# Kernel optimization log

Hardware: AMD Instinct MI355X
Metric: run time of the kernel (lower is better)

## Reference

```python
import jax, jax.numpy as jnp
import numpy as np

PARENT_LIST = [0, 0, 1, 2, 3, 4, 5, 6, 7, 8, 8, 3, 11, 12, 13, 14, 15, 15, 0, 18, 19, 20, 0, 22, 23, 24, 3]
J, D, H, L, DFF = 27, 512, 8, 6, 2048
DH = D // H
RADIUS = 0.1
B, N = 64, 2048
NEG = -1e9  # large finite negative: exp underflows to exactly 0 in fp32, grad-safe


def _topo_mask():
    m = np.full((J, J), NEG, dtype=np.float32)
    for c, p in enumerate(PARENT_LIST):
        m[c, c] = 0.0
        if c != p:
            m[c, p] = 0.0
            m[p, c] = 0.0
    return jnp.asarray(m)


def _radius_scales():
    s = np.ones(J, dtype=np.float32)
    s[[0, 1, 2, 3, 18, 22]] = 0.6
    s[[9, 10, 16, 17, 20, 21, 24, 25, 26]] = 1.5
    return jnp.asarray(s).reshape(1, J, 1)


def _ln(x, s, b):
    mu = jnp.mean(x, -1, keepdims=True)
    v = jnp.mean((x - mu) ** 2, -1, keepdims=True)
    return (x - mu) * jax.lax.rsqrt(v + 1e-5) * s + b


def _mha(q_in, k_in, v_in, qkv_w, qkv_b, out_w, out_b, add_mask):
    Bq, Q, _ = q_in.shape
    S = k_in.shape[1]
    q = (q_in @ qkv_w[:, :D] + qkv_b[:D]).reshape(Bq, Q, H, DH)
    k = (k_in @ qkv_w[:, D:2 * D] + qkv_b[D:2 * D]).reshape(Bq, S, H, DH)
    v = (v_in @ qkv_w[:, 2 * D:] + qkv_b[2 * D:]).reshape(Bq, S, H, DH)
    scores = jnp.einsum('bqhd,bkhd->bhqk', q, k) * np.float32(1.0 / np.sqrt(DH))
    attn = jax.nn.softmax(scores + add_mask, axis=-1)
    o = jnp.einsum('bhqk,bkhd->bqhd', attn, v).reshape(Bq, Q, D)
    return o @ out_w + out_b


def setup_inputs() -> dict:
    key = jax.random.key(0)
    ks = iter(jax.random.split(key, 40))
    def w(shape, scale=0.02):
        return jax.random.normal(next(ks), shape, jnp.float32) * scale
    return dict(
        x_t=jax.random.normal(next(ks), (B, J, 3), jnp.float32),
        t=jax.random.uniform(next(ks), (B, 1), jnp.float32),
        coarse_pose=jax.random.normal(next(ks), (B, J, 3), jnp.float32),
        radar_pc=jax.random.normal(next(ks), (B, N, 6), jnp.float32),
        pc_w=w((6, D)), pc_b=jnp.zeros(D),
        coarse_w=w((3, D)), coarse_b=jnp.zeros(D),
        state_w=w((3, D)), state_b=jnp.zeros(D),
        jid_emb=w((J, D), 1.0),
        dop_w1=w((1, 64)), dop_b1=jnp.zeros(64),
        dop_w2=w((64, D)), dop_b2=jnp.zeros(D),
        time_w1=w((1, D)), time_b1=jnp.zeros(D),
        time_w2=w((D, D)), time_b2=jnp.zeros(D),
        mod_w1=w((D, 2 * D)), mod_b1=jnp.zeros(2 * D),
        mod_w2=w((2 * D, 2 * D)), mod_b2=jnp.zeros(2 * D),
        diff_w=w((2 * D, D)), diff_b=jnp.zeros(D),
        vel_w=w((D, 3)), vel_b=jnp.zeros(3),
        sa_qkv_w=w((L, D, 3 * D)), sa_qkv_b=jnp.zeros((L, 3 * D)),
        sa_out_w=w((L, D, D)), sa_out_b=jnp.zeros((L, D)),
        ca_qkv_w=w((L, D, 3 * D)), ca_qkv_b=jnp.zeros((L, 3 * D)),
        ca_out_w=w((L, D, D)), ca_out_b=jnp.zeros((L, D)),
        ff1_w=w((L, D, DFF)), ff1_b=jnp.zeros((L, DFF)),
        ff2_w=w((L, DFF, D)), ff2_b=jnp.zeros((L, D)),
        ln1_s=jnp.ones((L, D)), ln1_b=jnp.zeros((L, D)),
        ln2_s=jnp.ones((L, D)), ln2_b=jnp.zeros((L, D)),
        ln3_s=jnp.ones((L, D)), ln3_b=jnp.zeros((L, D)),
    )


def reference(x_t, t, coarse_pose, radar_pc, pc_w, pc_b, coarse_w, coarse_b,
              state_w, state_b, jid_emb, dop_w1, dop_b1, dop_w2, dop_b2,
              time_w1, time_b1, time_w2, time_b2, mod_w1, mod_b1, mod_w2, mod_b2,
              diff_w, diff_b, vel_w, vel_b,
              sa_qkv_w, sa_qkv_b, sa_out_w, sa_out_b,
              ca_qkv_w, ca_qkv_b, ca_out_w, ca_out_b,
              ff1_w, ff1_b, ff2_w, ff2_b,
              ln1_s, ln1_b, ln2_s, ln2_b, ln3_s, ln3_b):
    p_idx = jnp.asarray(PARENT_LIST)
    topo = _topo_mask()          # [J,J] additive
    scales = _radius_scales()    # [1,J,1]
    pc_xyz = radar_pc[:, :, :3]
    pc_dop = radar_pc[:, :, 3:4]
    raw_memory = radar_pc @ pc_w + pc_b                               # [B,N,D]
    # euclidean distance via norm expansion (cdist p=2)
    d2 = (jnp.sum(x_t ** 2, -1)[:, :, None] + jnp.sum(pc_xyz ** 2, -1)[:, None, :]
          - 2.0 * jnp.einsum('bjc,bnc->bjn', x_t, pc_xyz))
    dist = jnp.sqrt(jnp.maximum(d2, 0.0))                             # [B,J,N]
    ar = scales * RADIUS                                              # [1,J,1]
    sig = ar / 2.0
    dw = jnp.exp(-dist ** 2 / (2.0 * sig ** 2))                       # [B,J,N]
    pi = jnp.max(dw, axis=1, keepdims=True)                           # [B,1,N]
    memory = raw_memory * jnp.swapaxes(pi, 1, 2)                      # [B,N,D]
    dop_feat = jax.nn.silu(pc_dop @ dop_w1 + dop_b1) @ dop_w2 + dop_b2
    denom = jnp.sum(dw, -1, keepdims=True) + 1e-6
    h_dop = jnp.einsum('bjn,bnd->bjd', dw, dop_feat) / denom
    h_coarse = coarse_pose @ coarse_w + coarse_b
    h_time = (jax.nn.silu(t @ time_w1 + time_b1) @ time_w2 + time_b2)[:, None, :]
    h_state = x_t @ state_w + state_b
    h_parent = h_state[:, p_idx, :]
    h_struct = jnp.concatenate([h_state, h_parent], -1) @ diff_w + diff_b
    query = h_coarse + h_time + h_dop + h_state + h_struct + jid_emb[None]
    mod = jax.nn.silu(h_state @ mod_w1 + mod_b1) @ mod_w2 + mod_b2
    shift, scale = jnp.split(mod, 2, axis=-1)
    query = query * (1.0 + scale) + shift
    # radius mask with nearest-point rescue
    smask = dist > ar
    min_idx = jnp.argmin(dist, axis=-1)                               # [B,J]
    rescue = jnp.arange(dist.shape[-1])[None, None, :] != min_idx[:, :, None]
    smask = jnp.where(jnp.all(smask, -1, keepdims=True), rescue, smask)
    mem_bias = jnp.where(smask, NEG, 0.0)[:, None, :, :]              # [B,1,J,N]
    tgt_bias = topo[None, None]                                       # [1,1,J,J]
    x = query
    for l in range(L):  # norm_first TransformerDecoderLayer, relu FFN, no dropout
        h = _ln(x, ln1_s[l], ln1_b[l])
        x = x + _mha(h, h, h, sa_qkv_w[l], sa_qkv_b[l], sa_out_w[l], sa_out_b[l], tgt_bias)
        h = _ln(x, ln2_s[l], ln2_b[l])
        x = x + _mha(h, memory, memory, ca_qkv_w[l], ca_qkv_b[l], ca_out_w[l], ca_out_b[l], mem_bias)
        h = _ln(x, ln3_s[l], ln3_b[l])
        x = x + jax.nn.relu(h @ ff1_w[l] + ff1_b[l]) @ ff2_w[l] + ff2_b[l]
    return x @ vel_w + vel_b
```

## Files before the change

kernel.cpp:

```cpp
#include <hip/hip_runtime.h>

#define J 27
#define D 512
#define H 8
#define DH 64
#define NLAYER 6
#define DFF 2048
#define NB 64
#define NP 2048
#define CAP 128
#define GCH 16
#define GPTS 128
#define NEGF -1000000000.0f

typedef unsigned short u16;
typedef __attribute__((ext_vector_type(8))) __bf16 bf16x8;
typedef __attribute__((ext_vector_type(4))) float f32x4;

__constant__ int c_parent[J] = {0,0,1,2,3,4,5,6,7,8,8,3,11,12,13,14,15,15,0,18,19,20,0,22,23,24,3};
__constant__ float c_scale[J] = {0.6f,0.6f,0.6f,0.6f,1.f,1.f,1.f,1.f,1.f,1.5f,1.5f,1.f,1.f,1.f,1.f,1.f,
                                 1.5f,1.5f,0.6f,1.f,1.5f,1.5f,0.6f,1.f,1.5f,1.5f,1.5f};

__device__ __forceinline__ float siluf(float x){ return x/(1.f+expf(-x)); }

__device__ __forceinline__ u16 f2bf(float f){
  union { float f; unsigned u; } x; x.f = f;
  unsigned r = x.u + 0x7FFFu + ((x.u >> 16) & 1u);
  return (u16)(r >> 16);
}

__global__ void k_perj(const float* __restrict__ x_t, const float* __restrict__ pc,
                       float* __restrict__ denom_sum, int* __restrict__ rescue,
                       int* __restrict__ allm, unsigned int* __restrict__ bitmap){
  int bj = blockIdx.x; int b = bj / J, j = bj % J;
  int t = threadIdx.x;
  float x0 = x_t[(b*J+j)*3+0];
  float x1 = x_t[(b*J+j)*3+1];
  float x2 = x_t[(b*J+j)*3+2];
  float sx = x0*x0+x1*x1+x2*x2;
  float ar = c_scale[j]*0.1f;
  float sig = ar*0.5f;
  float twos2 = 2.f*sig*sig;
  float sum = 0.f, bmin = 3.4e38f; int bidx = NP; int any = 0;
  for (int n = t; n < NP; n += 256){
    const float* p = pc + ((size_t)b*NP + n)*6;
    float p0=p[0], p1=p[1], p2=p[2];
    float d2 = sx + (p0*p0+p1*p1+p2*p2) - 2.f*(x0*p0+x1*p1+x2*p2);
    float dist = sqrtf(fmaxf(d2, 0.f));
    sum += expf(-(dist*dist)/twos2);
    if (dist < bmin){ bmin = dist; bidx = n; }
    if (dist <= ar){ any = 1; atomicOr(&bitmap[b*(NP/32)+(n>>5)], 1u<<(n&31)); }
  }
  __shared__ float ssum[256]; __shared__ float smin[256];
  __shared__ int sidx[256]; __shared__ int sany[256];
  ssum[t]=sum; smin[t]=bmin; sidx[t]=bidx; sany[t]=any;
  __syncthreads();
  for (int s = 128; s > 0; s >>= 1){
    if (t < s){
      ssum[t] += ssum[t+s];
      if (smin[t+s] < smin[t] || (smin[t+s]==smin[t] && sidx[t+s] < sidx[t])){ smin[t]=smin[t+s]; sidx[t]=sidx[t+s]; }
      sany[t] |= sany[t+s];
    }
    __syncthreads();
  }
  if (t == 0){
    denom_sum[bj] = ssum[0];
    rescue[bj] = sidx[0];
    allm[bj] = sany[0] ? 0 : 1;
    if (!sany[0]) atomicOr(&bitmap[b*(NP/32)+(sidx[0]>>5)], 1u<<(sidx[0]&31));
  }
}

__global__ void k_compact(const unsigned int* __restrict__ bitmap, int* __restrict__ act_idx,
                          int* __restrict__ act_cnt){
  int b = blockIdx.x; int t = threadIdx.x;
  unsigned int w = bitmap[b*(NP/32)+t];
  int c = __popc(w);
  int off = c;
  for (int s = 1; s < 64; s <<= 1){
    int v = __shfl_up(off, s);
    if (t >= s) off += v;
  }
  int total = __shfl(off, 63);
  off -= c;
  int base = off;
  for (int bit = 0; bit < 32; ++bit){
    if (w & (1u<<bit)){
      if (base < CAP) act_idx[b*CAP+base] = t*32+bit;
      base++;
    }
  }
  if (t == 0) act_cnt[b] = total > CAP ? CAP : total;
}

__global__ void k_scan(const int* __restrict__ act_cnt, int* __restrict__ act_off,
                       int* __restrict__ act_total){
  if (threadIdx.x == 0){
    int s = 0;
    for (int b = 0; b < NB; ++b){ act_off[b] = s; s += act_cnt[b]; }
    act_total[0] = s;
  }
}

__launch_bounds__(256)
__global__ void k_gpart(const float* __restrict__ x_t, const float* __restrict__ pc,
                        const float* __restrict__ dop_w1, const float* __restrict__ dop_b1,
                        float* __restrict__ Gp){
  int b = blockIdx.x, ch = blockIdx.y; int t = threadIdx.x;
  __shared__ float sx[J*3];
  __shared__ float w1s[64], b1s[64];
  __shared__ float spx[GPTS], spy[GPTS], spz[GPTS], sdp[GPTS];
  __shared__ u16 hidT[64*128];
  __shared__ u16 dwsA[32*128];
  if (t < J*3) sx[t] = x_t[b*J*3 + t];
  if (t < 64){ w1s[t] = dop_w1[t]; b1s[t] = dop_b1[t]; }
  int n0 = ch*GPTS;
  if (t < GPTS){
    const float* p = pc + ((size_t)b*NP + n0 + t)*6;
    float2 f0 = *(const float2*)p;
    float2 f1 = *(const float2*)(p+2);
    spx[t]=f0.x; spy[t]=f0.y; spz[t]=f1.x; sdp[t]=f1.y;
  }
  __syncthreads();
  {
    int h = t & 63, pb = (t>>6)*32;
    float w1 = w1s[h], b1 = b1s[h];
    char* base = (char*)hidT;
    #pragma unroll
    for (int m = 0; m < 16; ++m){
      float v0 = siluf(sdp[pb+2*m]*w1 + b1);
      float v1 = siluf(sdp[pb+2*m+1]*w1 + b1);
      unsigned pk = (unsigned)f2bf(v0) | ((unsigned)f2bf(v1) << 16);
      int off = (h*256 + pb*2 + 4*m) ^ ((h&7)<<4);
      *(unsigned*)(base + off) = pk;
    }
  }
  {
    int j = t & 31, pb = (t>>5)*16;
    if (j < J){
      float x0=sx[j*3], x1=sx[j*3+1], x2=sx[j*3+2];
      float sxx = x0*x0+x1*x1+x2*x2;
      float sig = c_scale[j]*0.05f;
      float inv2 = 1.f/(2.f*sig*sig);
      char* base = (char*)dwsA;
      #pragma unroll
      for (int m = 0; m < 8; ++m){
        float v[2];
        #pragma unroll
        for (int u = 0; u < 2; ++u){
          int p = pb + 2*m + u;
          float p0=spx[p], p1=spy[p], p2=spz[p];
          float d2 = sxx + (p0*p0+p1*p1+p2*p2) - 2.f*(x0*p0+x1*p1+x2*p2);
          float dist = sqrtf(fmaxf(d2, 0.f));
          v[u] = expf(-(dist*dist)*inv2);
        }
        unsigned pk = (unsigned)f2bf(v[0]) | ((unsigned)f2bf(v[1]) << 16);
        int off = (j*256 + pb*2 + 4*m) ^ ((j&7)<<4);
        *(unsigned*)(base + off) = pk;
      }
    }
  }
  __syncthreads();
  int lane = t & 63, wv = t >> 6;
  int h0 = wv * 16;
  int fr = lane & 15, fkb = (lane>>4)*16;
  f32x4 acc[2] = {};
  #pragma unroll
  for (int ks = 0; ks < 4; ++ks){
    bf16x8 bfrag;
    {
      int row = h0 + fr;
      int adr = (row*256 + ks*64 + fkb) ^ ((row&7)<<4);
      bfrag = *(const bf16x8*)((char*)hidT + adr);
    }
    #pragma unroll
    for (int m = 0; m < 2; ++m){
      int row = m*16 + fr;
      int adr = (row*256 + ks*64 + fkb) ^ ((row&7)<<4);
      bf16x8 afrag = *(const bf16x8*)((char*)dwsA + adr);
      acc[m] = __builtin_amdgcn_mfma_f32_16x16x32_bf16(afrag, bfrag, acc[m], 0,0,0);
    }
  }
  float* out = Gp + ((size_t)(b*GCH+ch))*J*64;
  int er = (lane>>4)*4, ec = lane&15;
  #pragma unroll
  for (int m = 0; m < 2; ++m){
    #pragma unroll
    for (int q = 0; q < 4; ++q){
      int j = m*16 + er + q;
      if (j < J) out[j*64 + h0 + ec] = acc[m][q];
    }
  }
}

__global__ void k_gred(const float* __restrict__ Gp, float* __restrict__ G){
  int idx = blockIdx.x*256 + threadIdx.x;
  int bj = idx >> 6, h = idx & 63;
  int b = bj / J, j = bj % J;
  float s = 0.f;
  #pragma unroll
  for (int c = 0; c < GCH; ++c) s += Gp[((size_t)(b*GCH+c)*J + j)*64 + h];
  G[idx] = s;
}

__launch_bounds__(256)
__global__ void k_hdop2(const float* __restrict__ G, const float* __restrict__ dop_w2,
                        const float* __restrict__ dop_b2, const float* __restrict__ denom_sum,
                        float* __restrict__ h_dop){
  int b = blockIdx.x, half = blockIdx.y;
  int t = threadIdx.x;
  int d = half*256 + t;
  __shared__ float sG[J*64];
  __shared__ float sS[J], sI[J];
  for (int e = t; e < J*64; e += 256) sG[e] = G[(size_t)b*J*64 + e];
  if (t < J){ float S = denom_sum[b*J+t]; sS[t] = S; sI[t] = 1.f/(S+1e-6f); }
  __syncthreads();
  float acc[J];
  #pragma unroll
  for (int j = 0; j < J; ++j) acc[j] = 0.f;
  for (int h = 0; h < 64; ++h){
    float wv = dop_w2[h*D + d];
    #pragma unroll
    for (int j = 0; j < J; ++j) acc[j] += sG[j*64+h]*wv;
  }
  float b2 = dop_b2[d];
  #pragma unroll
  for (int j = 0; j < J; ++j)
    h_dop[(size_t)(b*J+j)*D + d] = (acc[j] + sS[j]*b2)*sI[j];
}

__global__ void k_stage1(const float* __restrict__ x_t, const float* __restrict__ state_w,
                         const float* __restrict__ state_b,
                         const float* __restrict__ coarse, const float* __restrict__ coarse_w,
                         const float* __restrict__ coarse_b,
                         const float* __restrict__ t_in, const float* __restrict__ time_w1,
                         const float* __restrict__ time_b1,
                         float* __restrict__ h_state, u16* __restrict__ hsh,
                         float* __restrict__ h_coarse, u16* __restrict__ thh){
  const int RD = NB*J*D;
  int idx = blockIdx.x*256 + threadIdx.x;
  if (idx < RD){
    int r = idx / D, d = idx % D;
    const float* ir = x_t + r*3;
    float v = ir[0]*state_w[d] + ir[1]*state_w[D+d] + ir[2]*state_w[2*D+d] + state_b[d];
    h_state[idx] = v;
    hsh[idx] = f2bf(v);
  } else if (idx < 2*RD){
    int k = idx - RD;
    int r = k / D, d = k % D;
    const float* ir = coarse + r*3;
    h_coarse[k] = ir[0]*coarse_w[d] + ir[1]*coarse_w[D+d] + ir[2]*coarse_w[2*D+d] + coarse_b[d];
  } else if (idx < 2*RD + NB*D){
    int k = idx - 2*RD;
    int b = k / D, d = k % D;
    float v = siluf(t_in[b]*time_w1[d] + time_b1[d]);
    thh[k] = f2bf(v);
  }
}

__global__ void k_hs2(const float* __restrict__ h_state, u16* __restrict__ oh){
  int idx = blockIdx.x*256 + threadIdx.x;
  if (idx >= NB*J*2*D) return;
  int r = idx / (2*D), c = idx % (2*D);
  int b = r / J, j = r % J;
  float v;
  if (c < D) v = h_state[(size_t)r*D + c];
  else       v = h_state[((size_t)(b*J) + c_parent[j])*D + (c-D)];
  oh[idx] = f2bf(v);
}

__global__ void k_query(const float* __restrict__ h_coarse, const float* __restrict__ h_time,
                        const float* __restrict__ h_dop, const float* __restrict__ h_state,
                        const float* __restrict__ hstruct, const float* __restrict__ jid,
                        const float* __restrict__ mod2, float* __restrict__ x){
  int idx = blockIdx.x*256 + threadIdx.x;
  if (idx >= NB*J*D) return;
  int r = idx / D, d = idx % D;
  int b = r / J, j = r % J;
  float q = h_coarse[idx] + h_time[b*D+d] + h_dop[idx] + h_state[idx] + hstruct[idx] + jid[j*D+d];
  float shift = mod2[(size_t)r*2*D + d];
  float scale = mod2[(size_t)r*2*D + D + d];
  x[idx] = q*(1.f+scale) + shift;
}

__global__ void k_memact(const float* __restrict__ x_t, const float* __restrict__ pc,
                         const float* __restrict__ pc_w, const float* __restrict__ pc_b,
                         const int* __restrict__ act_idx, const int* __restrict__ act_cnt,
                         const int* __restrict__ act_off, u16* __restrict__ mh){
  int b = blockIdx.x / CAP, i = blockIdx.x % CAP;
  if (i >= act_cnt[b]) return;
  int n = act_idx[b*CAP+i];
  int t = threadIdx.x;
  __shared__ float sdw[J];
  __shared__ float spi;
  const float* p = pc + ((size_t)b*NP+n)*6;
  if (t < J){
    float x0 = x_t[(b*J+t)*3+0], x1 = x_t[(b*J+t)*3+1], x2 = x_t[(b*J+t)*3+2];
    float p0=p[0], p1=p[1], p2=p[2];
    float d2 = (x0*x0+x1*x1+x2*x2) + (p0*p0+p1*p1+p2*p2) - 2.f*(x0*p0+x1*p1+x2*p2);
    float dist = sqrtf(fmaxf(d2,0.f));
    float sig = c_scale[t]*0.05f;
    sdw[t] = expf(-(dist*dist)/(2.f*sig*sig));
  }
  __syncthreads();
  if (t == 0){ float m = sdw[0]; for (int k = 1; k < J; ++k) m = fmaxf(m, sdw[k]); spi = m; }
  __syncthreads();
  float pi = spi;
  float p0=p[0],p1=p[1],p2=p[2],p3=p[3],p4=p[4],p5=p[5];
  int g = act_off[b] + i;
  for (int d = t; d < D; d += 128){
    float acc = pc_b[d] + p0*pc_w[d] + p1*pc_w[D+d] + p2*pc_w[2*D+d]
              + p3*pc_w[3*D+d] + p4*pc_w[4*D+d] + p5*pc_w[5*D+d];
    mh[(size_t)g*D + d] = f2bf(acc * pi);
  }
}

__launch_bounds__(256)
__global__ void k_wconv(const float* __restrict__ W, u16* __restrict__ Wt, int K, int N){
  int k0 = blockIdx.x*64, n0 = blockIdx.y*64;
  size_t zo = (size_t)blockIdx.z*K*N;
  __shared__ float tile[64][65];
  int t = threadIdx.x;
  #pragma unroll
  for (int i = 0; i < 16; ++i){
    int idx = i*256 + t; int k = idx>>6, n = idx&63;
    tile[k][n] = W[zo + (size_t)(k0+k)*N + n0+n];
  }
  __syncthreads();
  #pragma unroll
  for (int i = 0; i < 8; ++i){
    int idx = i*256 + t; int n = idx>>5, kp = (idx&31)*2;
    unsigned pk = (unsigned)f2bf(tile[kp][n]) | ((unsigned)f2bf(tile[kp+1][n])<<16);
    *(unsigned*)&Wt[zo + (size_t)(n0+n)*K + k0+kp] = pk;
  }
}

template<int TM>
__launch_bounds__(256)
__global__ void k_gemm(const u16* __restrict__ Ag, const u16* __restrict__ Bt,
                       const float* __restrict__ bias, const float* __restrict__ res,
                       float* __restrict__ Cf, u16* __restrict__ Ch,
                       int M, int N, int K, int act,
                       const int* __restrict__ Mdev, int ntx){
  int Meff = Mdev ? *Mdev : M;
  int nwg = gridDim.x;
  int q8 = nwg>>3, r8 = nwg&7;
  int xcd = blockIdx.x&7, loc = blockIdx.x>>3;
  int wg = (xcd < r8 ? xcd*(q8+1) : r8*(q8+1)+(xcd-r8)*q8) + loc;
  int row0 = (wg % ntx)*TM, col0 = (wg / ntx)*64;
  if (row0 >= Meff) return;

  constexpr int MFR = TM/32;
  constexpr int RW  = TM/2;
  __shared__ u16 sA[TM*64], sB[64*64];
  int t = threadIdx.x;
  int lane = t&63, w = t>>6, wr = w>>1, wc = w&1;
  int sm = t>>3, kc = t&7;
  const u16* pA1 = Ag + (size_t)(row0+sm)*K + kc*8;
  const u16* pA2 = (TM==64) ? Ag + (size_t)(row0+sm+32)*K + kc*8 : pA1;
  const u16* pB1 = Bt + (size_t)(col0+sm)*K + kc*8;
  const u16* pB2 = Bt + (size_t)(col0+sm+32)*K + kc*8;
  int o1 = (sm*128 + kc*16) ^ ((sm&7)<<4);
  int o2 = ((sm+32)*128 + kc*16) ^ ((sm&7)<<4);
  uint4 ra1, ra2, rb1, rb2;
  auto gload = [&](int kt){
    ra1 = *(const uint4*)(pA1 + kt);
    if constexpr (TM==64) ra2 = *(const uint4*)(pA2 + kt);
    rb1 = *(const uint4*)(pB1 + kt);
    rb2 = *(const uint4*)(pB2 + kt);
  };
  auto stage = [&](){
    *(uint4*)((char*)sA + o1) = ra1;
    if constexpr (TM==64) *(uint4*)((char*)sA + o2) = ra2;
    *(uint4*)((char*)sB + o1) = rb1;
    *(uint4*)((char*)sB + o2) = rb2;
  };
  int fr = lane&15, fkb = (lane>>4)*16;
  f32x4 acc[MFR][2] = {};
  gload(0);
  stage();
  __syncthreads();
  for (int kt = 0; kt < K; kt += 64){
    bool nxt = kt + 64 < K;
    if (nxt) gload(kt + 64);
    #pragma unroll
    for (int kk = 0; kk < 2; ++kk){
      bf16x8 af[MFR], bf[2];
      #pragma unroll
      for (int m = 0; m < MFR; ++m){
        int row = wr*RW + m*16 + fr;
        int adr = (row*128 + kk*64 + fkb) ^ ((row&7)<<4);
        af[m] = *(const bf16x8*)((char*)sA + adr);
      }
      #pragma unroll
      for (int n = 0; n < 2; ++n){
        int rowb = wc*32 + n*16 + fr;
        int adr = (rowb*128 + kk*64 + fkb) ^ ((rowb&7)<<4);
        bf[n] = *(const bf16x8*)((char*)sB + adr);
      }
      #pragma unroll
      for (int m = 0; m < MFR; ++m)
        #pragma unroll
        for (int n = 0; n < 2; ++n)
          acc[m][n] = __builtin_amdgcn_mfma_f32_16x16x32_bf16(af[m], bf[n], acc[m][n], 0,0,0);
    }
    if (nxt){
      __syncthreads();
      stage();
      __syncthreads();
    }
  }
  int er = (lane>>4)*4, ec = lane&15;
  #pragma unroll
  for (int m = 0; m < MFR; ++m){
    #pragma unroll
    for (int qq = 0; qq < 4; ++qq){
      int r = row0 + wr*RW + m*16 + er + qq;
      if (r >= Meff) continue;
      #pragma unroll
      for (int n = 0; n < 2; ++n){
        int c = col0 + wc*32 + n*16 + ec;
        float v = acc[m][n][qq] + bias[c];
        if (res) v += res[(size_t)r*N + c];
        if (act == 1) v = v/(1.f+expf(-v));
        else if (act == 2) v = fmaxf(v, 0.f);
        if (Cf) Cf[(size_t)r*N + c] = v;
        if (Ch) Ch[(size_t)r*N + c] = f2bf(v);
      }
    }
  }
}

__global__ void k_ln(const float* __restrict__ x, const float* __restrict__ s,
                     const float* __restrict__ bb, u16* __restrict__ oh){
  int r = blockIdx.x; int t = threadIdx.x;
  const float* xr = x + (size_t)r*D;
  float v0 = xr[t], v1 = xr[t+256];
  __shared__ float red[256];
  red[t] = v0+v1; __syncthreads();
  for (int st = 128; st > 0; st >>= 1){ if (t < st) red[t] += red[t+st]; __syncthreads(); }
  float mu = red[0]/(float)D;
  __syncthreads();
  float d0 = v0-mu, d1 = v1-mu;
  red[t] = d0*d0 + d1*d1; __syncthreads();
  for (int st = 128; st > 0; st >>= 1){ if (t < st) red[t] += red[t+st]; __syncthreads(); }
  float var = red[0]/(float)D;
  float rs = rsqrtf(var + 1e-5f);
  oh[(size_t)r*D + t]       = f2bf(d0*rs*s[t]       + bb[t]);
  oh[(size_t)r*D + t + 256] = f2bf(d1*rs*s[t+256]   + bb[t+256]);
}

__launch_bounds__(256)
__global__ void k_selfattn(const float* __restrict__ qkv, u16* __restrict__ oh){
  int bh = blockIdx.x; int b = bh / H, h = bh % H;
  int t = threadIdx.x;
  __shared__ float qs[J*DH], ks[J*DH], vs[J*DH];
  __shared__ float ss[J*J];
  for (int e = t; e < J*DH; e += 256){
    int j = e/DH, d = e%DH;
    const float* base = qkv + (size_t)(b*J+j)*1536 + h*DH + d;
    qs[e] = base[0]; ks[e] = base[512]; vs[e] = base[1024];
  }
  __syncthreads();
  for (int e = t; e < J*J; e += 256){
    int qj = e/J, kk = e%J;
    float acc = 0.f;
    for (int d = 0; d < DH; ++d) acc += qs[qj*DH+d]*ks[kk*DH+d];
    float bias = (qj==kk || c_parent[qj]==kk || c_parent[kk]==qj) ? 0.f : NEGF;
    ss[e] = acc*0.125f + bias;
  }
  __syncthreads();
  if (t < J){
    float m = -3.4e38f;
    for (int k = 0; k < J; ++k) m = fmaxf(m, ss[t*J+k]);
    float sum = 0.f;
    for (int k = 0; k < J; ++k){ float e_ = expf(ss[t*J+k]-m); ss[t*J+k] = e_; sum += e_; }
    float inv = 1.f/sum;
    for (int k = 0; k < J; ++k) ss[t*J+k] *= inv;
  }
  __syncthreads();
  for (int e = t; e < J*DH; e += 256){
    int j = e/DH, d = e%DH;
    float acc = 0.f;
    for (int k = 0; k < J; ++k) acc += ss[j*J+k]*vs[k*DH+d];
    oh[(size_t)(b*J+j)*D + h*DH + d] = f2bf(acc);
  }
}

__launch_bounds__(256)
__global__ void k_crossattn(const float* __restrict__ qbuf, const float* __restrict__ kv_act,
                            const float* __restrict__ x_t, const float* __restrict__ pc,
                            const int* __restrict__ act_idx, const int* __restrict__ act_cnt,
                            const int* __restrict__ act_off, const int* __restrict__ rescue,
                            const int* __restrict__ allm, u16* __restrict__ oh){
  int bh = blockIdx.x; int b = bh / H, h = bh % H;
  int t = threadIdx.x;
  int cnt = act_cnt[b], off = act_off[b];
  __shared__ float qs[J*DH];
  __shared__ float ks[CAP*DH];
  __shared__ float pxyz[CAP*3];
  __shared__ float sx[J*3];
  __shared__ int sn[CAP];
  __shared__ float ss[J*CAP];
  if (t < J*3) sx[t] = x_t[b*J*3+t];
  for (int e = t; e < J*DH; e += 256)
    qs[e] = qbuf[(size_t)(b*J + e/DH)*D + h*DH + (e%DH)];
  for (int e = t; e < cnt*DH; e += 256){
    int i = e/DH, d = e%DH;
    ks[e] = kv_act[(size_t)(off+i)*1024 + h*DH + d];
  }
  for (int i = t; i < cnt; i += 256){
    int n = act_idx[b*CAP+i]; sn[i] = n;
    const float* p = pc + ((size_t)b*NP+n)*6;
    pxyz[i*3] = p[0]; pxyz[i*3+1] = p[1]; pxyz[i*3+2] = p[2];
  }
  __syncthreads();
  for (int e = t; e < J*cnt; e += 256){
    int j = e/cnt, i = e%cnt;
    float acc = 0.f;
    for (int d = 0; d < DH; ++d) acc += qs[j*DH+d]*ks[i*DH+d];
    float bias;
    if (allm[b*J+j]) bias = (sn[i] == rescue[b*J+j]) ? 0.f : NEGF;
    else {
      float x0=sx[j*3], x1=sx[j*3+1], x2=sx[j*3+2];
      float p0=pxyz[i*3], p1=pxyz[i*3+1], p2=pxyz[i*3+2];
      float d2 = (x0*x0+x1*x1+x2*x2) + (p0*p0+p1*p1+p2*p2) - 2.f*(x0*p0+x1*p1+x2*p2);
      float dist = sqrtf(fmaxf(d2,0.f));
      float ar = c_scale[j]*0.1f;
      bias = (dist > ar) ? NEGF : 0.f;
    }
    ss[j*CAP+i] = acc*0.125f + bias;
  }
  __syncthreads();
  if (t < J){
    float m = -3.4e38f;
    for (int i = 0; i < cnt; ++i) m = fmaxf(m, ss[t*CAP+i]);
    float sum = 0.f;
    for (int i = 0; i < cnt; ++i){ float e_ = expf(ss[t*CAP+i]-m); ss[t*CAP+i] = e_; sum += e_; }
    float inv = 1.f/sum;
    for (int i = 0; i < cnt; ++i) ss[t*CAP+i] *= inv;
  }
  __syncthreads();
  for (int e = t; e < J*DH; e += 256){
    int j = e/DH, d = e%DH;
    float acc = 0.f;
    for (int i = 0; i < cnt; ++i)
      acc += ss[j*CAP+i]*kv_act[(size_t)(off+i)*1024 + 512 + h*DH + d];
    oh[(size_t)(b*J+j)*D + h*DH + d] = f2bf(acc);
  }
}

__global__ void k_vel(const float* __restrict__ x, const float* __restrict__ vel_w,
                      const float* __restrict__ vel_b, float* __restrict__ out){
  int r = blockIdx.x; int t = threadIdx.x;
  int c = t >> 6; int lane = t & 63;
  float acc = 0.f;
  const float* xr = x + (size_t)r*D;
  for (int d = lane; d < D; d += 64) acc += xr[d]*vel_w[d*3+c];
  for (int s = 32; s > 0; s >>= 1) acc += __shfl_down(acc, s);
  if (lane == 0) out[r*3+c] = acc + vel_b[c];
}

static void gemm(const u16* Ah, const u16* Bt, const float* bias,
                 const float* res, float* Cf, u16* Ch,
                 int M, int N, int K, int act, const int* Mdev, int tm, hipStream_t s){
  if (tm == 32){
    int ntx = (M + 31) / 32;
    k_gemm<32><<<ntx*(N/64), 256, 0, s>>>(Ah, Bt, bias, res, Cf, Ch, M, N, K, act, Mdev, ntx);
  } else {
    int ntx = (M + 63) / 64;
    k_gemm<64><<<ntx*(N/64), 256, 0, s>>>(Ah, Bt, bias, res, Cf, Ch, M, N, K, act, Mdev, ntx);
  }
}

extern "C" void kernel_launch(void* const* d_in, const int* in_sizes, int n_in,
                              void* d_out, int out_size, void* d_ws, size_t ws_size,
                              hipStream_t stream){
  const float* x_t        = (const float*)d_in[0];
  const float* t_in       = (const float*)d_in[1];
  const float* coarse     = (const float*)d_in[2];
  const float* radar      = (const float*)d_in[3];
  const float* pc_w       = (const float*)d_in[4];
  const float* pc_b       = (const float*)d_in[5];
  const float* coarse_w   = (const float*)d_in[6];
  const float* coarse_b   = (const float*)d_in[7];
  const float* state_w    = (const float*)d_in[8];
  const float* state_b    = (const float*)d_in[9];
  const float* jid_emb    = (const float*)d_in[10];
  const float* dop_w1     = (const float*)d_in[11];
  const float* dop_b1     = (const float*)d_in[12];
  const float* dop_w2     = (const float*)d_in[13];
  const float* dop_b2     = (const float*)d_in[14];
  const float* time_w1    = (const float*)d_in[15];
  const float* time_b1    = (const float*)d_in[16];
  const float* time_w2    = (const float*)d_in[17];
  const float* time_b2    = (const float*)d_in[18];
  const float* mod_w1     = (const float*)d_in[19];
  const float* mod_b1     = (const float*)d_in[20];
  const float* mod_w2     = (const float*)d_in[21];
  const float* mod_b2     = (const float*)d_in[22];
  const float* diff_w     = (const float*)d_in[23];
  const float* diff_b     = (const float*)d_in[24];
  const float* vel_w      = (const float*)d_in[25];
  const float* vel_b      = (const float*)d_in[26];
  const float* sa_qkv_w   = (const float*)d_in[27];
  const float* sa_qkv_b   = (const float*)d_in[28];
  const float* sa_out_w   = (const float*)d_in[29];
  const float* sa_out_b   = (const float*)d_in[30];
  const float* ca_qkv_w   = (const float*)d_in[31];
  const float* ca_qkv_b   = (const float*)d_in[32];
  const float* ca_out_w   = (const float*)d_in[33];
  const float* ca_out_b   = (const float*)d_in[34];
  const float* ff1_w      = (const float*)d_in[35];
  const float* ff1_b      = (const float*)d_in[36];
  const float* ff2_w      = (const float*)d_in[37];
  const float* ff2_b      = (const float*)d_in[38];
  const float* ln1_s      = (const float*)d_in[39];
  const float* ln1_b      = (const float*)d_in[40];
  const float* ln2_s      = (const float*)d_in[41];
  const float* ln2_b      = (const float*)d_in[42];
  const float* ln3_s      = (const float*)d_in[43];
  const float* ln3_b      = (const float*)d_in[44];
  (void)in_sizes; (void)n_in; (void)out_size; (void)ws_size;

  const int R = NB*J;

  char* wp = (char*)d_ws;
  auto alloc = [&](size_t bytes)->void*{
    void* r = (void*)wp;
    wp += (bytes + 255) & ~(size_t)255;
    return r;
  };
  float*        denom_sum = (float*)alloc(R*4);
  int*          rescue    = (int*)  alloc(R*4);
  int*          allm      = (int*)  alloc(R*4);
  unsigned int* bitmap    = (unsigned int*)alloc(NB*(NP/32)*4);
  int*          act_idx   = (int*)  alloc(NB*CAP*4);
  int*          act_cnt   = (int*)  alloc(NB*4);
  int*          act_off   = (int*)  alloc(NB*4);
  int*          act_total = (int*)  alloc(64);
  float* Gp       = (float*)alloc((size_t)NB*GCH*J*64*4);
  float* G        = (float*)alloc((size_t)R*64*4);
  float* h_dop    = (float*)alloc((size_t)R*D*4);
  float* h_state  = (float*)alloc((size_t)R*D*4);
  float* h_coarse = (float*)alloc((size_t)R*D*4);
  float* hstruct  = (float*)alloc((size_t)R*D*4);
  float* xres     = (float*)alloc((size_t)R*D*4);
  float* qbuf     = (float*)alloc((size_t)R*D*4);
  float* h_time   = (float*)alloc((size_t)NB*D*4);
  float* mod2     = (float*)alloc((size_t)R*2*D*4);
  float* qkv      = (float*)alloc((size_t)R*3*D*4);
  float* kv_act   = (float*)alloc((size_t)NB*CAP*2*D*4);
  u16* hsh   = (u16*)alloc((size_t)R*D*2);
  u16* hbufh = (u16*)alloc((size_t)R*D*2);
  u16* attnoh= (u16*)alloc((size_t)R*D*2);
  u16* ffhh  = (u16*)alloc((size_t)R*DFF*2);
  u16* mah   = (u16*)alloc((size_t)NB*CAP*D*2);
  u16* time_w2t = (u16*)alloc((size_t)512*512*2);
  u16* mod_w1t  = (u16*)alloc((size_t)1024*512*2);
  u16* mod_w2t  = (u16*)alloc((size_t)1024*1024*2);
  u16* diff_wt  = (u16*)alloc((size_t)512*1024*2);
  u16* sa_qkv_t = (u16*)alloc((size_t)NLAYER*1536*512*2);
  u16* sa_out_t = (u16*)alloc((size_t)NLAYER*512*512*2);
  u16* ca_qkv_t = (u16*)alloc((size_t)NLAYER*1536*512*2);
  u16* ca_out_t = (u16*)alloc((size_t)NLAYER*512*512*2);
  u16* ff1_t    = (u16*)alloc((size_t)NLAYER*2048*512*2);
  u16* ff2_t    = (u16*)alloc((size_t)NLAYER*512*2048*2);
  u16* thh   = attnoh;
  u16* mod1h = ffhh;
  u16* hs2h  = (u16*)kv_act;

  k_wconv<<<dim3(8, 8, 1),  256, 0, stream>>>(time_w2, time_w2t, 512, 512);
  k_wconv<<<dim3(8, 16, 1), 256, 0, stream>>>(mod_w1, mod_w1t, 512, 1024);
  k_wconv<<<dim3(16, 16, 1),256, 0, stream>>>(mod_w2, mod_w2t, 1024, 1024);
  k_wconv<<<dim3(16, 8, 1), 256, 0, stream>>>(diff_w, diff_wt, 1024, 512);
  k_wconv<<<dim3(8, 24, NLAYER), 256, 0, stream>>>(sa_qkv_w, sa_qkv_t, 512, 1536);
  k_wconv<<<dim3(8, 8, NLAYER),  256, 0, stream>>>(sa_out_w, sa_out_t, 512, 512);
  k_wconv<<<dim3(8, 24, NLAYER), 256, 0, stream>>>(ca_qkv_w, ca_qkv_t, 512, 1536);
  k_wconv<<<dim3(8, 8, NLAYER),  256, 0, stream>>>(ca_out_w, ca_out_t, 512, 512);
  k_wconv<<<dim3(8, 32, NLAYER), 256, 0, stream>>>(ff1_w, ff1_t, 512, 2048);
  k_wconv<<<dim3(32, 8, NLAYER), 256, 0, stream>>>(ff2_w, ff2_t, 2048, 512);

  hipMemsetAsync(bitmap, 0, NB*(NP/32)*4, stream);
  k_perj<<<R, 256, 0, stream>>>(x_t, radar, denom_sum, rescue, allm, bitmap);
  k_compact<<<NB, 64, 0, stream>>>(bitmap, act_idx, act_cnt);
  k_scan<<<1, 64, 0, stream>>>(act_cnt, act_off, act_total);
  k_gpart<<<dim3(NB, GCH), 256, 0, stream>>>(x_t, radar, dop_w1, dop_b1, Gp);
  k_gred<<<R*64/256, 256, 0, stream>>>(Gp, G);
  k_hdop2<<<dim3(NB, 2), 256, 0, stream>>>(G, dop_w2, dop_b2, denom_sum, h_dop);

  k_stage1<<<(2*R*D + NB*D + 255)/256, 256, 0, stream>>>(
      x_t, state_w, state_b, coarse, coarse_w, coarse_b, t_in, time_w1, time_b1,
      h_state, hsh, h_coarse, thh);
  gemm(thh, time_w2t, time_b2, nullptr, h_time, nullptr, NB, 512, 512, 0, nullptr, 32, stream);
  gemm(hsh, mod_w1t, mod_b1, nullptr, nullptr, mod1h, R, 1024, 512, 1, nullptr, 32, stream);
  gemm(mod1h, mod_w2t, mod_b2, nullptr, mod2, nullptr, R, 1024, 1024, 0, nullptr, 32, stream);
  k_hs2<<<(R*2*D+255)/256, 256, 0, stream>>>(h_state, hs2h);
  gemm(hs2h, diff_wt, diff_b, nullptr, hstruct, nullptr, R, 512, 1024, 0, nullptr, 32, stream);
  k_query<<<(R*D+255)/256, 256, 0, stream>>>(h_coarse, h_time, h_dop, h_state, hstruct,
                                             jid_emb, mod2, xres);
  k_memact<<<NB*CAP, 128, 0, stream>>>(x_t, radar, pc_w, pc_b, act_idx, act_cnt, act_off, mah);

  for (int l = 0; l < NLAYER; ++l){
    k_ln<<<R, 256, 0, stream>>>(xres, ln1_s + l*D, ln1_b + l*D, hbufh);
    gemm(hbufh, sa_qkv_t + (size_t)l*1536*512, sa_qkv_b + l*1536, nullptr,
         qkv, nullptr, R, 1536, 512, 0, nullptr, 32, stream);
    k_selfattn<<<NB*H, 256, 0, stream>>>(qkv, attnoh);
    gemm(attnoh, sa_out_t + (size_t)l*512*512, sa_out_b + l*D, xres,
         xres, nullptr, R, 512, 512, 0, nullptr, 32, stream);

    k_ln<<<R, 256, 0, stream>>>(xres, ln2_s + l*D, ln2_b + l*D, hbufh);
    gemm(hbufh, ca_qkv_t + (size_t)l*1536*512, ca_qkv_b + l*1536, nullptr,
         qbuf, nullptr, R, 512, 512, 0, nullptr, 32, stream);
    gemm(mah, ca_qkv_t + (size_t)l*1536*512 + (size_t)512*512, ca_qkv_b + l*1536 + 512,
         nullptr, kv_act, nullptr, NB*CAP, 1024, 512, 0, act_total, 64, stream);
    k_crossattn<<<NB*H, 256, 0, stream>>>(qbuf, kv_act, x_t, radar, act_idx, act_cnt,
                                          act_off, rescue, allm, attnoh);
    gemm(attnoh, ca_out_t + (size_t)l*512*512, ca_out_b + l*D, xres,
         xres, nullptr, R, 512, 512, 0, nullptr, 32, stream);

    k_ln<<<R, 256, 0, stream>>>(xres, ln3_s + l*D, ln3_b + l*D, hbufh);
    gemm(hbufh, ff1_t + (size_t)l*2048*512, ff1_b + l*DFF, nullptr,
         nullptr, ffhh, R, 2048, 512, 2, nullptr, 32, stream);
    gemm(ffhh, ff2_t + (size_t)l*512*2048, ff2_b + l*D, xres,
         xres, nullptr, R, 512, 2048, 0, nullptr, 32, stream);
  }

  k_vel<<<R, 192, 0, stream>>>(xres, vel_w, vel_b, (float*)d_out);
}
```

Before: 1.062 ms.

## Double-buffer GEMM LDS, fuse small launches, merge cross-attn projections

The GEMM kernel now double-buffers its LDS tiles, which removes one barrier per K-step so the next tile's store overlaps the current MFMA work. The ten weight-conversion launches become one table-driven kernel, and the Gp reduction is folded into k_hdop2, which drops a launch and a temporary buffer. The cross-attention Q projection and the KV projection run in a single dual-GEMM launch. The self-attention QKV and FF1 GEMMs switch to 64-row tiles. LDS use per GEMM block doubles, which may reduce occupancy.

```diff
diff --git a/kernel.cpp b/kernel.cpp
--- a/kernel.cpp
+++ b/kernel.cpp
@@ -193,18 +193,8 @@
   }
 }
 
-__global__ void k_gred(const float* __restrict__ Gp, float* __restrict__ G){
-  int idx = blockIdx.x*256 + threadIdx.x;
-  int bj = idx >> 6, h = idx & 63;
-  int b = bj / J, j = bj % J;
-  float s = 0.f;
-  #pragma unroll
-  for (int c = 0; c < GCH; ++c) s += Gp[((size_t)(b*GCH+c)*J + j)*64 + h];
-  G[idx] = s;
-}
-
 __launch_bounds__(256)
-__global__ void k_hdop2(const float* __restrict__ G, const float* __restrict__ dop_w2,
+__global__ void k_hdop2(const float* __restrict__ Gp, const float* __restrict__ dop_w2,
                         const float* __restrict__ dop_b2, const float* __restrict__ denom_sum,
                         float* __restrict__ h_dop){
   int b = blockIdx.x, half = blockIdx.y;
@@ -212,7 +202,12 @@
   int d = half*256 + t;
   __shared__ float sG[J*64];
   __shared__ float sS[J], sI[J];
-  for (int e = t; e < J*64; e += 256) sG[e] = G[(size_t)b*J*64 + e];
+  for (int e = t; e < J*64; e += 256){
+    float s = 0.f;
+    #pragma unroll
+    for (int c = 0; c < GCH; ++c) s += Gp[(size_t)(b*GCH+c)*J*64 + e];
+    sG[e] = s;
+  }
   if (t < J){ float S = denom_sum[b*J+t]; sS[t] = S; sI[t] = 1.f/(S+1e-6f); }
   __syncthreads();
   float acc[J];
@@ -315,51 +310,63 @@
   }
 }
 
+struct WcD { const float* src; u16* dst; int K; int N; int tk; int tn; int L; int start; };
+struct WcTab { WcD d[10]; };
 __launch_bounds__(256)
-__global__ void k_wconv(const float* __restrict__ W, u16* __restrict__ Wt, int K, int N){
-  int k0 = blockIdx.x*64, n0 = blockIdx.y*64;
-  size_t zo = (size_t)blockIdx.z*K*N;
+__global__ void k_wconv_all(WcTab tab){
+  int tid = blockIdx.x;
+  WcD w = tab.d[0];
+  #pragma unroll
+  for (int i = 0; i < 10; ++i){
+    int end = tab.d[i].start + tab.d[i].tk*tab.d[i].tn*tab.d[i].L;
+    if (tid >= tab.d[i].start && tid < end) w = tab.d[i];
+  }
+  int local = tid - w.start;
+  int per = w.tk*w.tn;
+  int l = local / per, rem = local % per;
+  int k0 = (rem % w.tk)*64, n0 = (rem / w.tk)*64;
+  size_t zo = (size_t)l*w.K*w.N;
   __shared__ float tile[64][65];
   int t = threadIdx.x;
   #pragma unroll
   for (int i = 0; i < 16; ++i){
     int idx = i*256 + t; int k = idx>>6, n = idx&63;
-    tile[k][n] = W[zo + (size_t)(k0+k)*N + n0+n];
+    tile[k][n] = w.src[zo + (size_t)(k0+k)*w.N + n0+n];
   }
   __syncthreads();
   #pragma unroll
   for (int i = 0; i < 8; ++i){
     int idx = i*256 + t; int n = idx>>5, kp = (idx&31)*2;
     unsigned pk = (unsigned)f2bf(tile[kp][n]) | ((unsigned)f2bf(tile[kp+1][n])<<16);
-    *(unsigned*)&Wt[zo + (size_t)(n0+n)*K + k0+kp] = pk;
-  }
-}
+    *(unsigned*)&w.dst[zo + (size_t)(n0+n)*w.K + k0+kp] = pk;
+  }
+}
+
+struct GemmArgs {
+  const u16* Ag; const u16* Bt; const float* bias; const float* res;
+  float* Cf; u16* Ch; int M, N, K, act; const int* Mdev; int ntx; int nwg;
+};
 
 template<int TM>
-__launch_bounds__(256)
-__global__ void k_gemm(const u16* __restrict__ Ag, const u16* __restrict__ Bt,
-                       const float* __restrict__ bias, const float* __restrict__ res,
-                       float* __restrict__ Cf, u16* __restrict__ Ch,
-                       int M, int N, int K, int act,
-                       const int* __restrict__ Mdev, int ntx){
-  int Meff = Mdev ? *Mdev : M;
-  int nwg = gridDim.x;
-  int q8 = nwg>>3, r8 = nwg&7;
-  int xcd = blockIdx.x&7, loc = blockIdx.x>>3;
+__device__ __forceinline__ void gemm_body(const GemmArgs g, int bid, char* smem){
+  int Meff = g.Mdev ? *g.Mdev : g.M;
+  int q8 = g.nwg>>3, r8 = g.nwg&7;
+  int xcd = bid&7, loc = bid>>3;
   int wg = (xcd < r8 ? xcd*(q8+1) : r8*(q8+1)+(xcd-r8)*q8) + loc;
-  int row0 = (wg % ntx)*TM, col0 = (wg / ntx)*64;
+  int row0 = (wg % g.ntx)*TM, col0 = (wg / g.ntx)*64;
   if (row0 >= Meff) return;
-
-  constexpr int MFR = TM/32;
-  constexpr int RW  = TM/2;
-  __shared__ u16 sA[TM*64], sB[64*64];
+  constexpr int ABUF = TM*64*2;
+  constexpr int BBUF = 64*64*2;
+  char* sAb[2] = { smem, smem + ABUF };
+  char* sBb[2] = { smem + 2*ABUF, smem + 2*ABUF + BBUF };
   int t = threadIdx.x;
   int lane = t&63, w = t>>6, wr = w>>1, wc = w&1;
   int sm = t>>3, kc = t&7;
-  const u16* pA1 = Ag + (size_t)(row0+sm)*K + kc*8;
-  const u16* pA2 = (TM==64) ? Ag + (size_t)(row0+sm+32)*K + kc*8 : pA1;
-  const u16* pB1 = Bt + (size_t)(col0+sm)*K + kc*8;
-  const u16* pB2 = Bt + (size_t)(col0+sm+32)*K + kc*8;
+  int K = g.K, N = g.N;
+  const u16* pA1 = g.Ag + (size_t)(row0+sm)*K + kc*8;
+  const u16* pA2 = (TM==64) ? g.Ag + (size_t)(row0+sm+32)*K + kc*8 : pA1;
+  const u16* pB1 = g.Bt + (size_t)(col0+sm)*K + kc*8;
+  const u16* pB2 = g.Bt + (size_t)(col0+sm+32)*K + kc*8;
   int o1 = (sm*128 + kc*16) ^ ((sm&7)<<4);
   int o2 = ((sm+32)*128 + kc*16) ^ ((sm&7)<<4);
   uint4 ra1, ra2, rb1, rb2;
@@ -369,17 +376,20 @@
     rb1 = *(const uint4*)(pB1 + kt);
     rb2 = *(const uint4*)(pB2 + kt);
   };
-  auto stage = [&](){
-    *(uint4*)((char*)sA + o1) = ra1;
-    if constexpr (TM==64) *(uint4*)((char*)sA + o2) = ra2;
-    *(uint4*)((char*)sB + o1) = rb1;
-    *(uint4*)((char*)sB + o2) = rb2;
+  auto stage = [&](int bf_){
+    *(uint4*)(sAb[bf_] + o1) = ra1;
+    if constexpr (TM==64) *(uint4*)(sAb[bf_] + o2) = ra2;
+    *(uint4*)(sBb[bf_] + o1) = rb1;
+    *(uint4*)(sBb[bf_] + o2) = rb2;
   };
+  constexpr int MFR = TM/32;
+  constexpr int RW  = TM/2;
   int fr = lane&15, fkb = (lane>>4)*16;
   f32x4 acc[MFR][2] = {};
   gload(0);
-  stage();
-  __syncthreads();
+  stage(0);
+  __syncthreads();
+  int cur = 0;
   for (int kt = 0; kt < K; kt += 64){
     bool nxt = kt + 64 < K;
     if (nxt) gload(kt + 64);
@@ -390,13 +400,13 @@
       for (int m = 0; m < MFR; ++m){
         int row = wr*RW + m*16 + fr;
         int adr = (row*128 + kk*64 + fkb) ^ ((row&7)<<4);
-        af[m] = *(const bf16x8*)((char*)sA + adr);
+        af[m] = *(const bf16x8*)(sAb[cur] + adr);
       }
       #pragma unroll
       for (int n = 0; n < 2; ++n){
         int rowb = wc*32 + n*16 + fr;
         int adr = (rowb*128 + kk*64 + fkb) ^ ((rowb&7)<<4);
-        bf[n] = *(const bf16x8*)((char*)sB + adr);
+        bf[n] = *(const bf16x8*)(sBb[cur] + adr);
       }
       #pragma unroll
       for (int m = 0; m < MFR; ++m)
@@ -405,9 +415,9 @@
           acc[m][n] = __builtin_amdgcn_mfma_f32_16x16x32_bf16(af[m], bf[n], acc[m][n], 0,0,0);
     }
     if (nxt){
+      stage(cur^1);
       __syncthreads();
-      stage();
-      __syncthreads();
+      cur ^= 1;
     }
   }
   int er = (lane>>4)*4, ec = lane&15;
@@ -420,15 +430,30 @@
       #pragma unroll
       for (int n = 0; n < 2; ++n){
         int c = col0 + wc*32 + n*16 + ec;
-        float v = acc[m][n][qq] + bias[c];
-        if (res) v += res[(size_t)r*N + c];
-        if (act == 1) v = v/(1.f+expf(-v));
-        else if (act == 2) v = fmaxf(v, 0.f);
-        if (Cf) Cf[(size_t)r*N + c] = v;
-        if (Ch) Ch[(size_t)r*N + c] = f2bf(v);
+        float v = acc[m][n][qq] + g.bias[c];
+        if (g.res) v += g.res[(size_t)r*N + c];
+        if (g.act == 1) v = v/(1.f+expf(-v));
+        else if (g.act == 2) v = fmaxf(v, 0.f);
+        if (g.Cf) g.Cf[(size_t)r*N + c] = v;
+        if (g.Ch) g.Ch[(size_t)r*N + c] = f2bf(v);
       }
     }
   }
+}
+
+template<int TM>
+__launch_bounds__(256)
+__global__ void k_gemm(GemmArgs g){
+  constexpr int SZ = 2*(TM*64*2) + 2*(64*64*2);
+  __shared__ __align__(16) char smem[SZ];
+  gemm_body<TM>(g, blockIdx.x, smem);
+}
+
+__launch_bounds__(256)
+__global__ void k_gemm_dual(GemmArgs ga, GemmArgs gb){
+  __shared__ __align__(16) char smem[32768];
+  if ((int)blockIdx.x < ga.nwg) gemm_body<32>(ga, blockIdx.x, smem);
+  else                          gemm_body<64>(gb, blockIdx.x - ga.nwg, smem);
 }
 
 __global__ void k_ln(const float* __restrict__ x, const float* __restrict__ s,
@@ -561,16 +586,11 @@
   if (lane == 0) out[r*3+c] = acc + vel_b[c];
 }
 
-static void gemm(const u16* Ah, const u16* Bt, const float* bias,
-                 const float* res, float* Cf, u16* Ch,
-                 int M, int N, int K, int act, const int* Mdev, int tm, hipStream_t s){
-  if (tm == 32){
-    int ntx = (M + 31) / 32;
-    k_gemm<32><<<ntx*(N/64), 256, 0, s>>>(Ah, Bt, bias, res, Cf, Ch, M, N, K, act, Mdev, ntx);
-  } else {
-    int ntx = (M + 63) / 64;
-    k_gemm<64><<<ntx*(N/64), 256, 0, s>>>(Ah, Bt, bias, res, Cf, Ch, M, N, K, act, Mdev, ntx);
-  }
+static GemmArgs mk(const u16* A, const u16* Bt, const float* bias, const float* res,
+                   float* Cf, u16* Ch, int M, int N, int K, int act, const int* Mdev, int TM){
+  GemmArgs g; g.Ag=A; g.Bt=Bt; g.bias=bias; g.res=res; g.Cf=Cf; g.Ch=Ch;
+  g.M=M; g.N=N; g.K=K; g.act=act; g.Mdev=Mdev;
+  g.ntx=(M+TM-1)/TM; g.nwg=g.ntx*(N/64); return g;
 }
 
 extern "C" void kernel_launch(void* const* d_in, const int* in_sizes, int n_in,
@@ -640,7 +660,6 @@
   int*          act_off   = (int*)  alloc(NB*4);
   int*          act_total = (int*)  alloc(64);
   float* Gp       = (float*)alloc((size_t)NB*GCH*J*64*4);
-  float* G        = (float*)alloc((size_t)R*64*4);
   float* h_dop    = (float*)alloc((size_t)R*D*4);
   float* h_state  = (float*)alloc((size_t)R*D*4);
   float* h_coarse = (float*)alloc((size_t)R*D*4);
@@ -670,60 +689,80 @@
   u16* mod1h = ffhh;
   u16* hs2h  = (u16*)kv_act;
 
-  k_wconv<<<dim3(8, 8, 1),  256, 0, stream>>>(time_w2, time_w2t, 512, 512);
-  k_wconv<<<dim3(8, 16, 1), 256, 0, stream>>>(mod_w1, mod_w1t, 512, 1024);
-  k_wconv<<<dim3(16, 16, 1),256, 0, stream>>>(mod_w2, mod_w2t, 1024, 1024);
-  k_wconv<<<dim3(16, 8, 1), 256, 0, stream>>>(diff_w, diff_wt, 1024, 512);
-  k_wconv<<<dim3(8, 24, NLAYER), 256, 0, stream>>>(sa_qkv_w, sa_qkv_t, 512, 1536);
-  k_wconv<<<dim3(8, 8, NLAYER),  256, 0, stream>>>(sa_out_w, sa_out_t, 512, 512);
-  k_wconv<<<dim3(8, 24, NLAYER), 256, 0, stream>>>(ca_qkv_w, ca_qkv_t, 512, 1536);
-  k_wconv<<<dim3(8, 8, NLAYER),  256, 0, stream>>>(ca_out_w, ca_out_t, 512, 512);
-  k_wconv<<<dim3(8, 32, NLAYER), 256, 0, stream>>>(ff1_w, ff1_t, 512, 2048);
-  k_wconv<<<dim3(32, 8, NLAYER), 256, 0, stream>>>(ff2_w, ff2_t, 2048, 512);
+  {
+    WcTab tab;
+    int s = 0;
+    auto set = [&](int i, const float* src, u16* dst, int K, int N, int L){
+      tab.d[i].src = src; tab.d[i].dst = dst; tab.d[i].K = K; tab.d[i].N = N;
+      tab.d[i].tk = K/64; tab.d[i].tn = N/64; tab.d[i].L = L; tab.d[i].start = s;
+      s += (K/64)*(N/64)*L;
+    };
+    set(0, time_w2, time_w2t, 512, 512, 1);
+    set(1, mod_w1,  mod_w1t,  512, 1024, 1);
+    set(2, mod_w2,  mod_w2t,  1024, 1024, 1);
+    set(3, diff_w,  diff_wt,  1024, 512, 1);
+    set(4, sa_qkv_w, sa_qkv_t, 512, 1536, NLAYER);
+    set(5, sa_out_w, sa_out_t, 512, 512, NLAYER);
+    set(6, ca_qkv_w, ca_qkv_t, 512, 1536, NLAYER);
+    set(7, ca_out_w, ca_out_t, 512, 512, NLAYER);
+    set(8, ff1_w,    ff1_t,    512, 2048, NLAYER);
+    set(9, ff2_w,    ff2_t,    2048, 512, NLAYER);
+    k_wconv_all<<<s, 256, 0, stream>>>(tab);
+  }
 
   hipMemsetAsync(bitmap, 0, NB*(NP/32)*4, stream);
   k_perj<<<R, 256, 0, stream>>>(x_t, radar, denom_sum, rescue, allm, bitmap);
   k_compact<<<NB, 64, 0, stream>>>(bitmap, act_idx, act_cnt);
   k_scan<<<1, 64, 0, stream>>>(act_cnt, act_off, act_total);
   k_gpart<<<dim3(NB, GCH), 256, 0, stream>>>(x_t, radar, dop_w1, dop_b1, Gp);
-  k_gred<<<R*64/256, 256, 0, stream>>>(Gp, G);
-  k_hdop2<<<dim3(NB, 2), 256, 0, stream>>>(G, dop_w2, dop_b2, denom_sum, h_dop);
+  k_hdop2<<<dim3(NB, 2), 256, 0, stream>>>(Gp, dop_w2, dop_b2, denom_sum, h_dop);
 
   k_stage1<<<(2*R*D + NB*D + 255)/256, 256, 0, stream>>>(
       x_t, state_w, state_b, coarse, coarse_w, coarse_b, t_in, time_w1, time_b1,
       h_state, hsh, h_coarse, thh);
-  gemm(thh, time_w2t, time_b2, nullptr, h_time, nullptr, NB, 512, 512, 0, nullptr, 32, stream);
-  gemm(hsh, mod_w1t, mod_b1, nullptr, nullptr, mod1h, R, 1024, 512, 1, nullptr, 32, stream);
-  gemm(mod1h, mod_w2t, mod_b2, nullptr, mod2, nullptr, R, 1024, 1024, 0, nullptr, 32, stream);
+  { GemmArgs g = mk(thh, time_w2t, time_b2, nullptr, h_time, nullptr, NB, 512, 512, 0, nullptr, 32);
+    k_gemm<32><<<g.nwg, 256, 0, stream>>>(g); }
+  { GemmArgs g = mk(hsh, mod_w1t, mod_b1, nullptr, nullptr, mod1h, R, 1024, 512, 1, nullptr, 32);
+    k_gemm<32><<<g.nwg, 256, 0, stream>>>(g); }
+  { GemmArgs g = mk(mod1h, mod_w2t, mod_b2, nullptr, mod2, nullptr, R, 1024, 1024, 0, nullptr, 32);
+    k_gemm<32><<<g.nwg, 256, 0, stream>>>(g); }
   k_hs2<<<(R*2*D+255)/256, 256, 0, stream>>>(h_state, hs2h);
-  gemm(hs2h, diff_wt, diff_b, nullptr, hstruct, nullptr, R, 512, 1024, 0, nullptr, 32, stream);
+  { GemmArgs g = mk(hs2h, diff_wt, diff_b, nullptr, hstruct, nullptr, R, 512, 1024, 0, nullptr, 32);
+    k_gemm<32><<<g.nwg, 256, 0, stream>>>(g); }
   k_query<<<(R*D+255)/256, 256, 0, stream>>>(h_coarse, h_time, h_dop, h_state, hstruct,
                                              jid_emb, mod2, xres);
   k_memact<<<NB*CAP, 128, 0, stream>>>(x_t, radar, pc_w, pc_b, act_idx, act_cnt, act_off, mah);
 
   for (int l = 0; l < NLAYER; ++l){
     k_ln<<<R, 256, 0, stream>>>(xres, ln1_s + l*D, ln1_b + l*D, hbufh);
-    gemm(hbufh, sa_qkv_t + (size_t)l*1536*512, sa_qkv_b + l*1536, nullptr,
-         qkv, nullptr, R, 1536, 512, 0, nullptr, 32, stream);
+    { GemmArgs g = mk(hbufh, sa_qkv_t + (size_t)l*1536*512, sa_qkv_b + l*1536, nullptr,
+                      qkv, nullptr, R, 1536, 512, 0, nullptr, 64);
+      k_gemm<64><<<g.nwg, 256, 0, stream>>>(g); }
     k_selfattn<<<NB*H, 256, 0, stream>>>(qkv, attnoh);
-    gemm(attnoh, sa_out_t + (size_t)l*512*512, sa_out_b + l*D, xres,
-         xres, nullptr, R, 512, 512, 0, nullptr, 32, stream);
+    { GemmArgs g = mk(attnoh, sa_out_t + (size_t)l*512*512, sa_out_b + l*D, xres,
+                      xres, nullptr, R, 512, 512, 0, nullptr, 32);
+      k_gemm<32><<<g.nwg, 256, 0, stream>>>(g); }
 
     k_ln<<<R, 256, 0, stream>>>(xres, ln2_s + l*D, ln2_b + l*D, hbufh);
-    gemm(hbufh, ca_qkv_t + (size_t)l*1536*512, ca_qkv_b + l*1536, nullptr,
-         qbuf, nullptr, R, 512, 512, 0, nullptr, 32, stream);
-    gemm(mah, ca_qkv_t + (size_t)l*1536*512 + (size_t)512*512, ca_qkv_b + l*1536 + 512,
-         nullptr, kv_act, nullptr, NB*CAP, 1024, 512, 0, act_total, 64, stream);
+    { GemmArgs ga = mk(hbufh, ca_qkv_t + (size_t)l*1536*512, ca_qkv_b + l*1536, nullptr,
+                       qbuf, nullptr, R, 512, 512, 0, nullptr, 32);
+      GemmArgs gb = mk(mah, ca_qkv_t + (size_t)l*1536*512 + (size_t)512*512,
+                       ca_qkv_b + l*1536 + 512, nullptr,
+                       kv_act, nullptr, NB*CAP, 1024, 512, 0, act_total, 64);
+      k_gemm_dual<<<ga.nwg + gb.nwg, 256, 0, stream>>>(ga, gb); }
     k_crossattn<<<NB*H, 256, 0, stream>>>(qbuf, kv_act, x_t, radar, act_idx, act_cnt,
                                           act_off, rescue, allm, attnoh);
-    gemm(attnoh, ca_out_t + (size_t)l*512*512, ca_out_b + l*D, xres,
-         xres, nullptr, R, 512, 512, 0, nullptr, 32, stream);
+    { GemmArgs g = mk(attnoh, ca_out_t + (size_t)l*512*512, ca_out_b + l*D, xres,
+                      xres, nullptr, R, 512, 512, 0, nullptr, 32);
+      k_gemm<32><<<g.nwg, 256, 0, stream>>>(g); }
 
     k_ln<<<R, 256, 0, stream>>>(xres, ln3_s + l*D, ln3_b + l*D, hbufh);
-    gemm(hbufh, ff1_t + (size_t)l*2048*512, ff1_b + l*DFF, nullptr,
-         nullptr, ffhh, R, 2048, 512, 2, nullptr, 32, stream);
-    gemm(ffhh, ff2_t + (size_t)l*512*2048, ff2_b + l*D, xres,
-         xres, nullptr, R, 512, 2048, 0, nullptr, 32, stream);
+    { GemmArgs g = mk(hbufh, ff1_t + (size_t)l*2048*512, ff1_b + l*DFF, nullptr,
+                      nullptr, ffhh, R, 2048, 512, 2, nullptr, 64);
+      k_gemm<64><<<g.nwg, 256, 0, stream>>>(g); }
+    { GemmArgs g = mk(ffhh, ff2_t + (size_t)l*512*2048, ff2_b + l*D, xres,
+                      xres, nullptr, R, 512, 2048, 0, nullptr, 32);
+      k_gemm<32><<<g.nwg, 256, 0, stream>>>(g); }
   }
 
   k_vel<<<R, 192, 0, stream>>>(xres, vel_w, vel_b, (float*)d_out);
```

Measured after the change: 1.256 ms. +18.3%, slower.
